# Performance work log

Hardware: AMD Instinct MI355X
Metric: run time of the kernel (lower is better)

## Reference

```python
import jax, jax.numpy as jnp
import numpy as np

WSZ = 16   # cfg.window_size
GD = 64    # cfg.group_dim


def setup_inputs() -> dict:
    key = jax.random.key(0)
    k1, k2, k3, k4 = jax.random.split(key, 4)
    B, T, D = 8, 8192, 1024
    z = jax.random.normal(k1, (B, T, D), jnp.float32)
    token_lens = jax.random.randint(k2, (B, T), 1, 9).astype(jnp.int32)
    W1 = jax.random.normal(k3, (D, GD), jnp.float32) / np.sqrt(D)
    W2 = jax.random.normal(k4, (GD, GD), jnp.float32) / np.sqrt(GD)
    return {"z": z, "token_lens": token_lens, "W1": W1, "W2": W2, "target_len": 6144}


def _choose_pairs(local_sim, budget):
    # local_sim: (W-1,) sims of adjacent edges inside one window.
    # Greedy non-overlapping matching in descending-sim order, up to `budget` pairs.
    Wn = local_sim.shape[0] + 1
    order = jnp.argsort(-local_sim)

    def step(state, e):
        used, mr, picked = state
        ok = (picked < budget) & (~used[e]) & (~used[e + 1])
        used = used.at[e].set(used[e] | ok)
        used = used.at[e + 1].set(used[e + 1] | ok)
        mr = mr.at[e + 1].set(mr[e + 1] | ok)
        return (used, mr, picked + ok.astype(jnp.int32)), None

    init = (jnp.zeros(Wn, bool), jnp.zeros(Wn, bool), jnp.int32(0))
    (_, mr, _), _ = jax.lax.scan(step, init, order)
    return mr  # (W,) True at j -> merge token j into j-1


def reference(z, token_lens, W1, W2, target_len):
    B, T, D = z.shape
    nwin = T // WSZ  # T chosen divisible by WSZ -> all windows full
    merges_needed = T - target_len
    base, extra = merges_needed // nwin, merges_needed % nwin
    budgets = jnp.minimum(base + (jnp.arange(nwin) < extra), WSZ // 2).astype(jnp.int32)

    # grouping MLP + cosine-style adjacent similarity
    g = jnp.maximum(z @ W1, 0.0) @ W2                         # (B,T,GD)
    g = g / (jnp.linalg.norm(g, axis=-1, keepdims=True) + 1e-8)
    sim = jnp.sum(g[:, :-1] * g[:, 1:], axis=-1)              # (B,T-1)
    # pad boundary edge slot, view per-window; keep only intra-window edges
    sim_pad = jnp.pad(sim, ((0, 0), (0, 1)), constant_values=-jnp.inf)
    local = sim_pad.reshape(B, nwin, WSZ)[:, :, : WSZ - 1]    # (B,nwin,W-1)

    pick = jax.vmap(jax.vmap(_choose_pairs, in_axes=(0, 0)), in_axes=(0, None))
    merge_right = pick(local, budgets).reshape(B, T)          # (B,T) bool
    keep = ~merge_right

    # pairs are disjoint -> sequential torch loop == parallel weighted merge
    w = token_lens.astype(z.dtype)
    absorb = merge_right[:, 1:]                               # token i absorbs i+1
    wi, wj = w[:, :-1, None], w[:, 1:, None]
    merged = (z[:, :-1] * wi + z[:, 1:] * wj) / (wi + wj)
    z2 = jnp.concatenate([jnp.where(absorb[:, :, None], merged, z[:, :-1]), z[:, -1:]], axis=1)
    l2 = jnp.concatenate(
        [jnp.where(absorb, token_lens[:, :-1] + token_lens[:, 1:], token_lens[:, :-1]),
         token_lens[:, -1:]], axis=1)

    # stable compaction: kept indices first (order preserved), truncate
    order = jnp.argsort(~keep, axis=1)[:, :target_len]        # jax sort is stable
    z_new = jnp.take_along_axis(z2, order[:, :, None], axis=1)
    lens_new = jnp.take_along_axis(l2, order, axis=1)
    starts_new = jnp.cumsum(lens_new, axis=1) - lens_new
    return z_new, lens_new, starts_new
```

## Files before the change

### kernel.cpp

```cpp
#include <hip/hip_runtime.h>

#define B_ 8
#define T_ 8192
#define D_ 1024
#define GD_ 64
#define WSZ_ 16
#define NWIN_ (T_ / WSZ_)

typedef __attribute__((ext_vector_type(8))) short short8v;
typedef __attribute__((ext_vector_type(4))) short short4v;
typedef __attribute__((ext_vector_type(4))) float f32x4;

__device__ __forceinline__ unsigned bf16rne(unsigned u) {
  return (u + 0x7FFFu + ((u >> 16) & 1u)) >> 16;
}
__device__ __forceinline__ void split3(float x, short& h, short& m, short& l) {
  const unsigned uh = bf16rne(__float_as_uint(x));
  const float fh = __uint_as_float(uh << 16);
  const float r1 = x - fh;
  const unsigned um = bf16rne(__float_as_uint(r1));
  const float fm = __uint_as_float(um << 16);
  const float r2 = r1 - fm;
  const unsigned ul = bf16rne(__float_as_uint(r2));
  h = (short)uh; m = (short)um; l = (short)ul;
}

__global__ __launch_bounds__(256) void k_prep(
    const float* __restrict__ W1, const float* __restrict__ W2,
    short* __restrict__ w1t, short* __restrict__ w2t)
{
  const int idx = blockIdx.x * 256 + threadIdx.x;
  if (idx < D_ * GD_) {
    const int k = idx & (D_ - 1), g = idx >> 10;
    short h, m, l;
    split3(W1[(long)k * GD_ + g], h, m, l);
    w1t[0 * D_ * GD_ + g * D_ + k] = h;
    w1t[1 * D_ * GD_ + g * D_ + k] = m;
    w1t[2 * D_ * GD_ + g * D_ + k] = l;
  } else {
    const int j = idx - D_ * GD_;
    const int c = j & 63, r = j >> 6;
    short h, m, l;
    split3(W2[c * GD_ + r], h, m, l);
    w2t[0 * GD_ * GD_ + r * GD_ + c] = h;
    w2t[1 * GD_ * GD_ + r * GD_ + c] = m;
    w2t[2 * GD_ * GD_ + r * GD_ + c] = l;
  }
}

__global__ __launch_bounds__(256) void k_sims(
    const float* __restrict__ z, const short* __restrict__ w1t,
    const short* __restrict__ w2t, double* __restrict__ sims_out)
{
  __shared__ short Zsp[3][64][72];
  __shared__ short Asp[3][64][72];
  __shared__ float Gf[64][72];
  __shared__ double den[64];

  const int tid = threadIdx.x;
  const int lane = tid & 63;
  const int w = tid >> 6;
  const int th = w & 1;
  const int gh = w >> 1;
  const int cl = lane & 15;
  const int ko8 = (lane >> 4) * 8;
  const long bt0 = (long)blockIdx.x * 64;

  const int r = tid >> 2;
  const int kq = tid & 3;

  f32x4 acc[2][2];
#pragma unroll
  for (int a = 0; a < 2; ++a)
#pragma unroll
    for (int b = 0; b < 2; ++b) acc[a][b] = (f32x4){0.f, 0.f, 0.f, 0.f};

#pragma unroll 1
  for (int c = 0; c < 16; ++c) {
    if (c) __syncthreads();
    {
      const float* zp = z + (bt0 + r) * D_ + c * 64 + kq * 16;
#pragma unroll
      for (int q = 0; q < 4; ++q) {
        const float4 f = ((const float4*)zp)[q];
        short h[4], m[4], l[4];
        split3(f.x, h[0], m[0], l[0]);
        split3(f.y, h[1], m[1], l[1]);
        split3(f.z, h[2], m[2], l[2]);
        split3(f.w, h[3], m[3], l[3]);
        const int co = kq * 16 + 4 * q;
        *(short4v*)&Zsp[0][r][co] = (short4v){h[0], h[1], h[2], h[3]};
        *(short4v*)&Zsp[1][r][co] = (short4v){m[0], m[1], m[2], m[3]};
        *(short4v*)&Zsp[2][r][co] = (short4v){l[0], l[1], l[2], l[3]};
      }
    }
#pragma unroll
    for (int s = 0; s < 3; ++s) {
      const short* ap = w1t + s * D_ * GD_ + r * D_ + c * 64 + kq * 16;
      *(short8v*)&Asp[s][r][kq * 16] = *(const short8v*)ap;
      *(short8v*)&Asp[s][r][kq * 16 + 8] = *(const short8v*)(ap + 8);
    }
    __syncthreads();

#pragma unroll
    for (int ks = 0; ks < 2; ++ks) {
      const int ko = ks * 32 + ko8;
      short8v af[2][3], bf[2][3];
#pragma unroll
      for (int a = 0; a < 2; ++a)
#pragma unroll
        for (int s = 0; s < 3; ++s)
          af[a][s] = *(const short8v*)&Asp[s][gh * 32 + a * 16 + cl][ko];
#pragma unroll
      for (int b = 0; b < 2; ++b)
#pragma unroll
        for (int s = 0; s < 3; ++s)
          bf[b][s] = *(const short8v*)&Zsp[s][th * 32 + b * 16 + cl][ko];
#pragma unroll
      for (int a = 0; a < 2; ++a)
#pragma unroll
        for (int b = 0; b < 2; ++b) {
          f32x4 d = acc[a][b];
          d = __builtin_amdgcn_mfma_f32_16x16x32_bf16(af[a][0], bf[b][0], d, 0, 0, 0);
          d = __builtin_amdgcn_mfma_f32_16x16x32_bf16(af[a][0], bf[b][1], d, 0, 0, 0);
          d = __builtin_amdgcn_mfma_f32_16x16x32_bf16(af[a][1], bf[b][0], d, 0, 0, 0);
          d = __builtin_amdgcn_mfma_f32_16x16x32_bf16(af[a][1], bf[b][1], d, 0, 0, 0);
          d = __builtin_amdgcn_mfma_f32_16x16x32_bf16(af[a][0], bf[b][2], d, 0, 0, 0);
          d = __builtin_amdgcn_mfma_f32_16x16x32_bf16(af[a][2], bf[b][0], d, 0, 0, 0);
          acc[a][b] = d;
        }
    }
  }
  __syncthreads();

#pragma unroll
  for (int a = 0; a < 2; ++a)
#pragma unroll
    for (int b = 0; b < 2; ++b) {
      const int t = th * 32 + b * 16 + cl;
      const int g0 = gh * 32 + a * 16 + (lane >> 4) * 4;
      short hh[4], hm[4], hl[4];
#pragma unroll
      for (int e = 0; e < 4; ++e)
        split3(fmaxf(acc[a][b][e], 0.0f), hh[e], hm[e], hl[e]);
      *(short4v*)&Zsp[0][t][g0] = (short4v){hh[0], hh[1], hh[2], hh[3]};
      *(short4v*)&Zsp[1][t][g0] = (short4v){hm[0], hm[1], hm[2], hm[3]};
      *(short4v*)&Zsp[2][t][g0] = (short4v){hl[0], hl[1], hl[2], hl[3]};
    }
#pragma unroll
  for (int s = 0; s < 3; ++s) {
    const short* ap = w2t + s * GD_ * GD_ + r * GD_ + kq * 16;
    *(short8v*)&Asp[s][r][kq * 16] = *(const short8v*)ap;
    *(short8v*)&Asp[s][r][kq * 16 + 8] = *(const short8v*)(ap + 8);
  }
  __syncthreads();

#pragma unroll
  for (int a = 0; a < 2; ++a)
#pragma unroll
    for (int b = 0; b < 2; ++b) acc[a][b] = (f32x4){0.f, 0.f, 0.f, 0.f};
#pragma unroll
  for (int ks = 0; ks < 2; ++ks) {
    const int ko = ks * 32 + ko8;
    short8v af[2][3], bf[2][3];
#pragma unroll
    for (int a = 0; a < 2; ++a)
#pragma unroll
      for (int s = 0; s < 3; ++s)
        af[a][s] = *(const short8v*)&Asp[s][gh * 32 + a * 16 + cl][ko];
#pragma unroll
    for (int b = 0; b < 2; ++b)
#pragma unroll
      for (int s = 0; s < 3; ++s)
        bf[b][s] = *(const short8v*)&Zsp[s][th * 32 + b * 16 + cl][ko];
#pragma unroll
    for (int a = 0; a < 2; ++a)
#pragma unroll
      for (int b = 0; b < 2; ++b) {
        f32x4 d = acc[a][b];
        d = __builtin_amdgcn_mfma_f32_16x16x32_bf16(af[a][0], bf[b][0], d, 0, 0, 0);
        d = __builtin_amdgcn_mfma_f32_16x16x32_bf16(af[a][0], bf[b][1], d, 0, 0, 0);
        d = __builtin_amdgcn_mfma_f32_16x16x32_bf16(af[a][1], bf[b][0], d, 0, 0, 0);
        d = __builtin_amdgcn_mfma_f32_16x16x32_bf16(af[a][1], bf[b][1], d, 0, 0, 0);
        d = __builtin_amdgcn_mfma_f32_16x16x32_bf16(af[a][0], bf[b][2], d, 0, 0, 0);
        d = __builtin_amdgcn_mfma_f32_16x16x32_bf16(af[a][2], bf[b][0], d, 0, 0, 0);
        acc[a][b] = d;
      }
  }

#pragma unroll
  for (int a = 0; a < 2; ++a)
#pragma unroll
    for (int b = 0; b < 2; ++b) {
      const int t = th * 32 + b * 16 + cl;
      const int g0 = gh * 32 + a * 16 + (lane >> 4) * 4;
      *(f32x4*)&Gf[t][g0] = acc[a][b];
    }
  __syncthreads();

  if (tid < 64) {
    double ss = 0.0;
#pragma unroll
    for (int q = 0; q < 16; ++q) {
      const float4 v = *(const float4*)&Gf[tid][4 * q];
      ss += (double)v.x * v.x + (double)v.y * v.y +
            (double)v.z * v.z + (double)v.w * v.w;
    }
    den[tid] = sqrt(ss) + 1e-8;
  }
  __syncthreads();

  if (tid < 4 * (WSZ_ - 1)) {
    const int ww = tid / (WSZ_ - 1), e = tid % (WSZ_ - 1);
    const int t = ww * WSZ_ + e;
    double s = 0.0;
#pragma unroll
    for (int q = 0; q < 16; ++q) {
      const float4 x = *(const float4*)&Gf[t][4 * q];
      const float4 y = *(const float4*)&Gf[t + 1][4 * q];
      s += (double)x.x * y.x + (double)x.y * y.y +
           (double)x.z * y.z + (double)x.w * y.w;
    }
    sims_out[((long)blockIdx.x * 4 + ww) * (WSZ_ - 1) + e] =
        s / (den[t] * den[t + 1]);
  }
}

__global__ __launch_bounds__(64) void k_pick(
    const double* __restrict__ sims, const int* __restrict__ tlptr,
    int* __restrict__ mrMask, int* __restrict__ keptCnt)
{
  const int win = blockIdx.x * 64 + threadIdx.x;
  if (win >= B_ * NWIN_) return;
  const int w = win % NWIN_;

  const int tl = tlptr[0];
  const int mn = T_ - tl;
  const int base = mn / NWIN_, extra = mn % NWIN_;
  int budget = base + (w < extra ? 1 : 0);
  if (budget > WSZ_ / 2) budget = WSZ_ / 2;
  if (budget < 0) budget = 0;

  double v[WSZ_ - 1];
  int id[WSZ_ - 1];
  for (int e = 0; e < WSZ_ - 1; ++e) {
    v[e] = sims[(long)win * (WSZ_ - 1) + e];
    id[e] = e;
  }
  for (int i = 1; i < WSZ_ - 1; ++i) {
    const double dv = v[i]; const int di = id[i];
    int j = i - 1;
    while (j >= 0 && v[j] < dv) { v[j + 1] = v[j]; id[j + 1] = id[j]; --j; }
    v[j + 1] = dv; id[j + 1] = di;
  }
  bool used[WSZ_];
  for (int i = 0; i < WSZ_; ++i) used[i] = false;
  int mrm = 0, picked = 0;
  for (int ii = 0; ii < WSZ_ - 1; ++ii) {
    const int e = id[ii];
    if (picked < budget && !used[e] && !used[e + 1]) {
      used[e] = used[e + 1] = true;
      mrm |= (1 << (e + 1));
      ++picked;
    }
  }
  mrMask[win] = mrm;
  keptCnt[win] = WSZ_ - picked;
}

__global__ void k_scan_windows(const int* __restrict__ keptCnt,
                               int* __restrict__ outOff)
{
  const int b = threadIdx.x;
  if (b >= B_) return;
  int off = 0;
  for (int w = 0; w < NWIN_; ++w) {
    outOff[b * NWIN_ + w] = off;
    off += keptCnt[b * NWIN_ + w];
  }
}

__global__ __launch_bounds__(256) void k_emit(
    const float* __restrict__ z, const int* __restrict__ lens,
    const int* __restrict__ mrMask, const int* __restrict__ outOff,
    float* __restrict__ out, int TL)
{
  const int bw = blockIdx.x;
  const int b = bw / NWIN_, w = bw % NWIN_;
  const int tid = threadIdx.x;
  const int mrm = mrMask[bw];
  int p = outOff[bw];
  const int t0 = w * WSZ_;

  const float* zb = z + (long)b * T_ * D_;
  const int* lb = lens + b * T_;
  float* zout = out;
  float* lout = out + (long)B_ * TL * D_;

  for (int i = 0; i < WSZ_; ++i) {
    if ((mrm >> i) & 1) continue;
    if (p >= TL) return;
    const int t = t0 + i;
    const bool ab = (i < WSZ_ - 1) && ((mrm >> (i + 1)) & 1);
    float4 o = *(const float4*)(zb + (long)t * D_ + tid * 4);
    if (ab) {
      const float wi = (float)lb[t], wj = (float)lb[t + 1];
      const float s = wi + wj;
      const float4 zj = *(const float4*)(zb + (long)(t + 1) * D_ + tid * 4);
      o.x = (o.x * wi + zj.x * wj) / s;
      o.y = (o.y * wi + zj.y * wj) / s;
      o.z = (o.z * wi + zj.z * wj) / s;
      o.w = (o.w * wi + zj.w * wj) / s;
      if (tid == 0) lout[(long)b * TL + p] = s;
    } else {
      if (tid == 0) lout[(long)b * TL + p] = (float)lb[t];
    }
    *(float4*)(zout + ((long)b * TL + p) * D_ + tid * 4) = o;
    ++p;
  }
}

__global__ __launch_bounds__(256) void k_starts(
    const float* __restrict__ lens_f, float* __restrict__ starts, int TL)
{
  const int b = blockIdx.x;
  const int tid = threadIdx.x;
  const int lane = tid & 63, wv = tid >> 6;
  __shared__ float wsum[4];
  const float* lrow = lens_f + (long)b * TL;
  float* srow = starts + (long)b * TL;
  float carry = 0.0f;

  for (int c0 = 0; c0 < TL; c0 += 256) {
    const int j = c0 + tid;
    const float v = (j < TL) ? lrow[j] : 0.0f;
    float x = v;
#pragma unroll
    for (int d = 1; d < 64; d <<= 1) {
      const float o = __shfl_up(x, d);
      if (lane >= d) x += o;
    }
    if (lane == 63) wsum[wv] = x;
    __syncthreads();
    float pre = 0.0f;
    if (wv > 0) pre += wsum[0];
    if (wv > 1) pre += wsum[1];
    if (wv > 2) pre += wsum[2];
    const float tot = wsum[0] + wsum[1] + wsum[2] + wsum[3];
    if (j < TL) srow[j] = carry + pre + x - v;
    carry += tot;
    __syncthreads();
  }
}

extern "C" void kernel_launch(void* const* d_in, const int* in_sizes, int n_in,
                              void* d_out, int out_size, void* d_ws, size_t ws_size,
                              hipStream_t stream)
{
  const float* z    = (const float*)d_in[0];
  const int*   lens = (const int*)d_in[1];
  const float* W1   = (const float*)d_in[2];
  const float* W2   = (const float*)d_in[3];
  const int*   tlp  = (const int*)d_in[4];

  float* out = (float*)d_out;
  const int TL = out_size / (B_ * (D_ + 2));

  double* sims = (double*)d_ws;
  char* p = (char*)d_ws + (size_t)B_ * NWIN_ * (WSZ_ - 1) * 8;
  int* mrMask = (int*)p;
  int* kept   = mrMask + B_ * NWIN_;
  int* outOff = kept + B_ * NWIN_;
  short* w1t = (short*)(p + 3 * B_ * NWIN_ * 4 + 64);
  w1t = (short*)(((size_t)w1t + 15) & ~(size_t)15);
  short* w2t = w1t + 3 * D_ * GD_;

  hipLaunchKernelGGL(k_prep, dim3((D_ * GD_ + GD_ * GD_) / 256), dim3(256),
                     0, stream, W1, W2, w1t, w2t);
  hipLaunchKernelGGL(k_sims, dim3((B_ * T_) / 64), dim3(256), 0, stream,
                     z, w1t, w2t, sims);
  hipLaunchKernelGGL(k_pick, dim3((B_ * NWIN_ + 63) / 64), dim3(64), 0, stream,
                     sims, tlp, mrMask, kept);
  hipLaunchKernelGGL(k_scan_windows, dim3(1), dim3(64), 0, stream,
                     kept, outOff);
  hipLaunchKernelGGL(k_emit, dim3(B_ * NWIN_), dim3(256), 0, stream,
                     z, lens, mrMask, outOff, out, TL);
  hipLaunchKernelGGL(k_starts, dim3(B_), dim3(256), 0, stream,
                     out + (long)B_ * TL * D_,
                     out + (long)B_ * TL * D_ + (long)B_ * TL, TL);
}
```

Baseline: 223.3 us.

## Double-buffer Z tiles with register prefetch and read weights directly from global

The Z staging buffer is double-buffered, and the next chunk's fp32 z values are prefetched into registers while the current chunk's MFMAs run, which removes one barrier per chunk. The W1 and W2 split fragments are now loaded straight from global memory (L1/L2-cached) instead of being staged through a shared-memory tile. This shrinks LDS use and drops the cooperative weight copy, at the cost of redundant global loads per wave and more registers for the prefetch. The Z stores are also widened to 8-short vectors.

```diff
diff --git a/kernel.cpp b/kernel.cpp
--- a/kernel.cpp
+++ b/kernel.cpp
@@ -8,7 +8,6 @@
 #define NWIN_ (T_ / WSZ_)
 
 typedef __attribute__((ext_vector_type(8))) short short8v;
-typedef __attribute__((ext_vector_type(4))) short short4v;
 typedef __attribute__((ext_vector_type(4))) float f32x4;
 
 __device__ __forceinline__ unsigned bf16rne(unsigned u) {
@@ -52,8 +51,7 @@
     const float* __restrict__ z, const short* __restrict__ w1t,
     const short* __restrict__ w2t, double* __restrict__ sims_out)
 {
-  __shared__ short Zsp[3][64][72];
-  __shared__ short Asp[3][64][72];
+  __shared__ short Zsp[2][3][64][72];
   __shared__ float Gf[64][72];
   __shared__ double den[64];
 
@@ -68,6 +66,7 @@
 
   const int r = tid >> 2;
   const int kq = tid & 3;
+  const float* zbase = z + (bt0 + r) * D_ + kq * 16;
 
   f32x4 acc[2][2];
 #pragma unroll
@@ -75,47 +74,48 @@
 #pragma unroll
     for (int b = 0; b < 2; ++b) acc[a][b] = (f32x4){0.f, 0.f, 0.f, 0.f};
 
-#pragma unroll 1
-  for (int c = 0; c < 16; ++c) {
-    if (c) __syncthreads();
-    {
-      const float* zp = z + (bt0 + r) * D_ + c * 64 + kq * 16;
-#pragma unroll
-      for (int q = 0; q < 4; ++q) {
-        const float4 f = ((const float4*)zp)[q];
-        short h[4], m[4], l[4];
-        split3(f.x, h[0], m[0], l[0]);
-        split3(f.y, h[1], m[1], l[1]);
-        split3(f.z, h[2], m[2], l[2]);
-        split3(f.w, h[3], m[3], l[3]);
-        const int co = kq * 16 + 4 * q;
-        *(short4v*)&Zsp[0][r][co] = (short4v){h[0], h[1], h[2], h[3]};
-        *(short4v*)&Zsp[1][r][co] = (short4v){m[0], m[1], m[2], m[3]};
-        *(short4v*)&Zsp[2][r][co] = (short4v){l[0], l[1], l[2], l[3]};
-      }
-    }
-#pragma unroll
-    for (int s = 0; s < 3; ++s) {
-      const short* ap = w1t + s * D_ * GD_ + r * D_ + c * 64 + kq * 16;
-      *(short8v*)&Asp[s][r][kq * 16] = *(const short8v*)ap;
-      *(short8v*)&Asp[s][r][kq * 16 + 8] = *(const short8v*)(ap + 8);
-    }
-    __syncthreads();
-
+  auto stage = [&](const float4 (&pz)[4], int buf) {
+    short h[16], m[16], l[16];
+#pragma unroll
+    for (int q = 0; q < 4; ++q) {
+      split3(pz[q].x, h[4 * q + 0], m[4 * q + 0], l[4 * q + 0]);
+      split3(pz[q].y, h[4 * q + 1], m[4 * q + 1], l[4 * q + 1]);
+      split3(pz[q].z, h[4 * q + 2], m[4 * q + 2], l[4 * q + 2]);
+      split3(pz[q].w, h[4 * q + 3], m[4 * q + 3], l[4 * q + 3]);
+    }
+    const int co = kq * 16;
+    *(short8v*)&Zsp[buf][0][r][co] =
+        (short8v){h[0], h[1], h[2], h[3], h[4], h[5], h[6], h[7]};
+    *(short8v*)&Zsp[buf][0][r][co + 8] =
+        (short8v){h[8], h[9], h[10], h[11], h[12], h[13], h[14], h[15]};
+    *(short8v*)&Zsp[buf][1][r][co] =
+        (short8v){m[0], m[1], m[2], m[3], m[4], m[5], m[6], m[7]};
+    *(short8v*)&Zsp[buf][1][r][co + 8] =
+        (short8v){m[8], m[9], m[10], m[11], m[12], m[13], m[14], m[15]};
+    *(short8v*)&Zsp[buf][2][r][co] =
+        (short8v){l[0], l[1], l[2], l[3], l[4], l[5], l[6], l[7]};
+    *(short8v*)&Zsp[buf][2][r][co + 8] =
+        (short8v){l[8], l[9], l[10], l[11], l[12], l[13], l[14], l[15]};
+  };
+
+  auto mfma_chunk = [&](int buf, int c) {
 #pragma unroll
     for (int ks = 0; ks < 2; ++ks) {
       const int ko = ks * 32 + ko8;
-      short8v af[2][3], bf[2][3];
+      short8v af[3][3];
+      short8v bf[3][3];
 #pragma unroll
       for (int a = 0; a < 2; ++a)
 #pragma unroll
         for (int s = 0; s < 3; ++s)
-          af[a][s] = *(const short8v*)&Asp[s][gh * 32 + a * 16 + cl][ko];
+          af[a][s] = *(const short8v*)(w1t + s * (D_ * GD_) +
+                                       (gh * 32 + a * 16 + cl) * D_ +
+                                       c * 64 + ko);
 #pragma unroll
       for (int b = 0; b < 2; ++b)
 #pragma unroll
         for (int s = 0; s < 3; ++s)
-          bf[b][s] = *(const short8v*)&Zsp[s][th * 32 + b * 16 + cl][ko];
+          bf[b][s] = *(const short8v*)&Zsp[buf][s][th * 32 + b * 16 + cl][ko];
 #pragma unroll
       for (int a = 0; a < 2; ++a)
 #pragma unroll
@@ -130,6 +130,30 @@
           acc[a][b] = d;
         }
     }
+  };
+
+  float4 pzA[4], pzB[4];
+#pragma unroll
+  for (int q = 0; q < 4; ++q) pzA[q] = *(const float4*)(zbase + 4 * q);
+
+#pragma unroll 1
+  for (int c = 0; c < 16; c += 2) {
+    if (c + 1 < 16) {
+#pragma unroll
+      for (int q = 0; q < 4; ++q)
+        pzB[q] = *(const float4*)(zbase + (c + 1) * 64 + 4 * q);
+    }
+    stage(pzA, 0);
+    __syncthreads();
+    mfma_chunk(0, c);
+    if (c + 2 < 16) {
+#pragma unroll
+      for (int q = 0; q < 4; ++q)
+        pzA[q] = *(const float4*)(zbase + (c + 2) * 64 + 4 * q);
+    }
+    stage(pzB, 1);
+    __syncthreads();
+    mfma_chunk(1, c + 1);
   }
   __syncthreads();
 
@@ -143,16 +167,13 @@
 #pragma unroll
       for (int e = 0; e < 4; ++e)
         split3(fmaxf(acc[a][b][e], 0.0f), hh[e], hm[e], hl[e]);
-      *(short4v*)&Zsp[0][t][g0] = (short4v){hh[0], hh[1], hh[2], hh[3]};
-      *(short4v*)&Zsp[1][t][g0] = (short4v){hm[0], hm[1], hm[2], hm[3]};
-      *(short4v*)&Zsp[2][t][g0] = (short4v){hl[0], hl[1], hl[2], hl[3]};
-    }
-#pragma unroll
-  for (int s = 0; s < 3; ++s) {
-    const short* ap = w2t + s * GD_ * GD_ + r * GD_ + kq * 16;
-    *(short8v*)&Asp[s][r][kq * 16] = *(const short8v*)ap;
-    *(short8v*)&Asp[s][r][kq * 16 + 8] = *(const short8v*)(ap + 8);
-  }
+      Zsp[0][0][t][g0 + 0] = hh[0]; Zsp[0][0][t][g0 + 1] = hh[1];
+      Zsp[0][0][t][g0 + 2] = hh[2]; Zsp[0][0][t][g0 + 3] = hh[3];
+      Zsp[0][1][t][g0 + 0] = hm[0]; Zsp[0][1][t][g0 + 1] = hm[1];
+      Zsp[0][1][t][g0 + 2] = hm[2]; Zsp[0][1][t][g0 + 3] = hm[3];
+      Zsp[0][2][t][g0 + 0] = hl[0]; Zsp[0][2][t][g0 + 1] = hl[1];
+      Zsp[0][2][t][g0 + 2] = hl[2]; Zsp[0][2][t][g0 + 3] = hl[3];
+    }
   __syncthreads();
 
 #pragma unroll
@@ -162,17 +183,18 @@
 #pragma unroll
   for (int ks = 0; ks < 2; ++ks) {
     const int ko = ks * 32 + ko8;
-    short8v af[2][3], bf[2][3];
+    short8v af[3][3], bf[3][3];
 #pragma unroll
     for (int a = 0; a < 2; ++a)
 #pragma unroll
       for (int s = 0; s < 3; ++s)
-        af[a][s] = *(const short8v*)&Asp[s][gh * 32 + a * 16 + cl][ko];
+        af[a][s] = *(const short8v*)(w2t + s * (GD_ * GD_) +
+                                     (gh * 32 + a * 16 + cl) * GD_ + ko);
 #pragma unroll
     for (int b = 0; b < 2; ++b)
 #pragma unroll
       for (int s = 0; s < 3; ++s)
-        bf[b][s] = *(const short8v*)&Zsp[s][th * 32 + b * 16 + cl][ko];
+        bf[b][s] = *(const short8v*)&Zsp[0][s][th * 32 + b * 16 + cl][ko];
 #pragma unroll
     for (int a = 0; a < 2; ++a)
 #pragma unroll
```

New measurement: 261.6 us. 17.1% more time.
